# Kernel tuning notes

Measured on AMD Instinct MI355X. Metric: run time of the kernel, lower is better.

## Reference

```python
import jax, jax.numpy as jnp
import numpy as np

NB_LAYERS, KSIZE = 4, 5
DILATIONS = [1, 2, 4, 8]
NEG_SLOPE = 0.1
BN_EPS = 1e-5


def _cont_conv(times, feats, mask, dilation, p):
    """One ContConv1d layer: causal gather of time-diffs -> kernel MLP -> weighted aggregate + skip + BN."""
    k1W, k1b, k2W, k2b, k3W, k3b, skipW, skipb, gamma, beta = p
    bs, L, Cin = feats.shape
    Cout = skipW.shape[1]
    lags = jnp.arange(KSIZE) * dilation                    # (K,) include_zero_lag=True -> lag 0 included
    idx = jnp.arange(L)[None, :] - lags[:, None]           # (K, L) causal neighbor indices
    valid = idx >= 0
    idx_c = jnp.clip(idx, 0, L - 1)
    g_times = times[:, idx_c]                              # (bs, K, L)
    g_feats = feats[:, idx_c, :]                           # (bs, K, L, Cin)
    g_mask = (mask[:, idx_c] & valid[None] & mask[:, None, :]).astype(feats.dtype)
    dt = (times[:, None, :] - g_times) * g_mask            # (bs, K, L) zeroed where invalid
    # kernel MLP: scalar time-diff -> (Cin, Cout) mixing matrix
    h = jax.nn.leaky_relu(dt[..., None] @ k1W + k1b, NEG_SLOPE)
    h = jax.nn.leaky_relu(h @ k2W + k2b, NEG_SLOPE)
    kv = (h @ k3W + k3b).reshape(bs, KSIZE, L, Cin, Cout) * g_mask[..., None, None]
    out = jnp.einsum('bklc,bklcd->bld', g_feats, kv)       # aggregate over taps and input channels
    out = out + feats @ skipW + skipb                      # 1x1-conv skip connection
    mu = out.mean((0, 1))                                  # BatchNorm1d (training-mode batch stats)
    var = out.var((0, 1))
    return (out - mu) * jax.lax.rsqrt(var + BN_EPS) * gamma + beta


def _ccnn_forward(event_times, event_types, emb, k1W, k1b, k2W, k2b, k3W, k3b, skipW, skipb, gamma, beta):
    bs = event_times.shape[0]
    emb = emb.at[0].set(0.0)                               # padding_idx = 0
    times = jnp.concatenate([jnp.zeros((bs, 1), event_times.dtype), event_times], axis=1)
    bos = jnp.full((bs, 1), jnp.max(event_types) + 1, dtype=event_types.dtype)
    types = jnp.concatenate([bos, event_types], axis=1)
    mask = times != 0                                      # BOS (t=0) masked, as in the original
    enc = emb[types]                                       # (bs, L+1, C)
    for i in range(NB_LAYERS):
        p = (k1W[i], k1b[i], k2W[i], k2b[i], k3W[i], k3b[i], skipW[i], skipb[i], gamma[i], beta[i])
        enc = jax.nn.leaky_relu(_cont_conv(times, enc, mask, DILATIONS[i], p), NEG_SLOPE)
    return enc


def setup_inputs() -> dict:
    key = jax.random.key(0)
    ks = jax.random.split(key, 12)
    bs, L, C, H, num_types = 8, 2048, 32, 16, 100
    s = 0.05
    gaps = jax.random.uniform(ks[0], (bs, L)) * 0.1 + 0.01
    times = jnp.cumsum(gaps, axis=1)                       # strictly increasing positive event times
    types = jax.random.randint(ks[1], (bs, L), 0, num_types) + 1   # 1..num_types
    pad = jnp.arange(L) >= int(0.9 * L)
    times = jnp.where(pad[None, :], 0.0, times).astype(jnp.float32)
    types = jnp.where(pad[None, :], 0, types).astype(jnp.int32)
    return {
        'event_times': times,
        'event_types': types,
        'emb': jax.random.normal(ks[2], (num_types + 2, C)) * s,
        'k1W': jax.random.normal(ks[3], (NB_LAYERS, 1, H)) * s,
        'k1b': jnp.zeros((NB_LAYERS, H)),
        'k2W': jax.random.normal(ks[4], (NB_LAYERS, H, H)) * s,
        'k2b': jnp.zeros((NB_LAYERS, H)),
        'k3W': jax.random.normal(ks[5], (NB_LAYERS, H, C * C)) * s,
        'k3b': jnp.zeros((NB_LAYERS, C * C)),
        'skipW': jax.random.normal(ks[6], (NB_LAYERS, C, C)) * s,
        'skipb': jnp.zeros((NB_LAYERS, C)),
        'gamma': jnp.ones((NB_LAYERS, C)),
        'beta': jnp.zeros((NB_LAYERS, C)),
    }


def reference(event_times, event_types, emb, k1W, k1b, k2W, k2b, k3W, k3b, skipW, skipb, gamma, beta):
    return _ccnn_forward(event_times, event_types, emb, k1W, k1b, k2W, k2b, k3W, k3b, skipW, skipb, gamma, beta)
```

## Files before the change

### kernel.cpp

```cpp
#include <hip/hip_runtime.h>
#include <stdint.h>

#define NB_LAYERS 4
#define KSIZE 5
#define BSZ 8
#define LIN 2048
#define LSEQ 2049
#define CCH 32
#define HCH 16
#define MROWS (BSZ*LSEQ)
#define NTILES ((MROWS+15)/16)
#define KDIM 576
#define NEG 0.1f
#define BNEPS 1e-5f
#define NWAVEMAX 256
#define CONVGRID 205
#define CONVBLK 320

typedef _Float16 h2v __attribute__((ext_vector_type(2)));
typedef _Float16 h8v __attribute__((ext_vector_type(8)));
typedef float    f4v __attribute__((ext_vector_type(4)));

union H8 { h8v v; h2v h[4]; };

static __device__ __forceinline__ h2v mkh2(float a, float b) {
  h2v r; r[0] = (_Float16)a; r[1] = (_Float16)b; return r;
}

__global__ __launch_bounds__(256) void prep_kernel(
    const float* __restrict__ k3W, const float* __restrict__ k3b,
    const float* __restrict__ skipW, _Float16* __restrict__ Wt,
    const int* __restrict__ types, int* __restrict__ wavemax,
    float* __restrict__ stats) {
  int id = blockIdx.x * blockDim.x + threadIdx.x;

  if (id < NB_LAYERS * 64) stats[id] = 0.f;

  if (id < BSZ * LIN) {
    int v = types[id];
#pragma unroll
    for (int off = 32; off; off >>= 1) v = max(v, __shfl_xor(v, off, 64));
    if ((threadIdx.x & 63) == 0) wavemax[id >> 6] = v;
  }

  {
    int layer = id / (CCH * KDIM);
    int rem = id % (CCH * KDIM);
    int n = rem / KDIM;
    int k = rem % KDIM;
    float val;
    if (k < 512)      { int h = k >> 5, c = k & 31; val = k3W[layer*16384 + h*1024 + c*32 + n]; }
    else if (k < 544) { int c = k - 512;            val = k3b[layer*1024 + c*32 + n]; }
    else              { int c = k - 544;            val = skipW[layer*1024 + c*32 + n]; }
    Wt[id] = (_Float16)val;
  }
}

template<int MODE>
__global__ __launch_bounds__(CONVBLK) void conv_kernel(
    const float* __restrict__ enc_in,
    const int*   __restrict__ types,
    const float* __restrict__ emb,
    const int*   __restrict__ wavemax,
    float* __restrict__ enc_out,
    const float* __restrict__ etimes,
    const float* __restrict__ k1Wp, const float* __restrict__ k1bp,
    const float* __restrict__ k2Wp, const float* __restrict__ k2bp,
    const _Float16* __restrict__ Wt,
    const float* __restrict__ stats_prev, float* __restrict__ stats_out,
    const float* __restrict__ gamma_prev, const float* __restrict__ beta_prev,
    int dil)
{
  __shared__ float sst[64];
  __shared__ alignas(16) float sW[304];
  __shared__ h8v swh[CONVBLK/64 * KSIZE * 16 * 2];

  const int tid  = threadIdx.x;
  const int lane = tid & 63;
  const int wv   = tid >> 6;
  const int m    = lane & 15;
  const int q    = lane >> 4;

  if (tid < 64) sst[tid] = 0.f;
  if (tid < 16) { sW[tid] = k1Wp[tid]; sW[16 + tid] = k1bp[tid]; sW[32 + tid] = k2bp[tid]; }
  if (tid >= 64 && tid < 64 + 256) sW[48 + tid - 64] = k2Wp[tid - 64];
  __syncthreads();

  float sc8[8], ob8[8];
  if (MODE == 1) {
    const float inv = 1.f / (float)MROWS;
#pragma unroll
    for (int j = 0; j < 8; j++) {
      int c = q * 8 + j;
      float mu = stats_prev[c] * inv;
      float var = stats_prev[32 + c] * inv - mu * mu;
      float sc = gamma_prev[c] * rsqrtf(var + BNEPS);
      sc8[j] = sc; ob8[j] = beta_prev[c] - mu * sc;
    }
  }

  const _Float16* wb0 = Wt + m * KDIM + q * 8;
  const _Float16* wb1 = Wt + (m + 16) * KDIM + q * 8;

  const int tile = blockIdx.x * (CONVBLK / 64) + wv;
  int row = tile * 16 + m;
  bool rvalid = row < MROWS;
  int rowc = min(row, MROWS - 1);
  int b = rowc / LSEQ, pos = rowc % LSEQ;
  float t_l = (pos == 0) ? 0.f : etimes[b * LIN + pos - 1];
  bool mask_l = rvalid && (t_l != 0.f);

  int bosv = 0;
  if (MODE == 0) {
    if (__ballot(pos == 0)) {
      const int4* wm = (const int4*)wavemax;
      int mx = 0;
#pragma unroll 4
      for (int i = 0; i < NWAVEMAX / 4; i++) {
        int4 v = wm[i];
        mx = max(mx, max(max(v.x, v.y), max(v.z, v.w)));
      }
      bosv = mx + 1;
    }
  }

  h2v fh[KSIZE][4];
  h2v fself[4];
  float Fb[8];
#pragma unroll
  for (int jj = 0; jj < 8; jj++) Fb[jj] = 0.f;

#pragma unroll
  for (int tap = 0; tap < KSIZE; tap++) {
    int j = pos - tap * dil;
    int jc = max(j, 0);
    float t_j = (jc == 0) ? 0.f : etimes[b * LIN + jc - 1];
    bool gm = mask_l && (j >= 0) && (t_j != 0.f);

    float fv[8];
    if (MODE == 0) {
      int tl = 0;
      if (jc > 0) tl = types[b * LIN + jc - 1];
      int t = (jc == 0) ? ((tap == 0) ? bosv : 0) : tl;
      const float* ep = emb + t * CCH + q * 8;
      float4 eA = *(const float4*)(ep);
      float4 eB = *(const float4*)(ep + 4);
      float zf = (t != 0) ? 1.f : 0.f;
      fv[0]=eA.x*zf; fv[1]=eA.y*zf; fv[2]=eA.z*zf; fv[3]=eA.w*zf;
      fv[4]=eB.x*zf; fv[5]=eB.y*zf; fv[6]=eB.z*zf; fv[7]=eB.w*zf;
    } else {
      const float* fp = enc_in + (b * LSEQ + jc) * CCH + q * 8;
      float4 fA = *(const float4*)(fp);
      float4 fB = *(const float4*)(fp + 4);
      fv[0]=fA.x; fv[1]=fA.y; fv[2]=fA.z; fv[3]=fA.w;
      fv[4]=fB.x; fv[5]=fB.y; fv[6]=fB.z; fv[7]=fB.w;
#pragma unroll
      for (int jj = 0; jj < 8; jj++) {
        float x = fmaf(fv[jj], sc8[jj], ob8[jj]);
        fv[jj] = fmaxf(x, NEG * x);
      }
    }

    if (tap == 0) {
      float rv = rvalid ? 1.f : 0.f;
#pragma unroll
      for (int p2 = 0; p2 < 4; p2++) fself[p2] = mkh2(fv[2*p2] * rv, fv[2*p2+1] * rv);
    }
    float g = gm ? 1.f : 0.f;
#pragma unroll
    for (int jj = 0; jj < 8; jj++) Fb[jj] += g * fv[jj];
#pragma unroll
    for (int p2 = 0; p2 < 4; p2++) fh[tap][p2] = mkh2(fv[2*p2], fv[2*p2+1]);
  }

#pragma unroll
  for (int rep = 0; rep < 2; rep++) {
    const int jt = rep ? (KSIZE - 1) : (lane >> 4);
    const bool act = rep ? (lane < 16) : true;
    int j2 = pos - jt * dil;
    int jc2 = max(j2, 0);
    float tj2 = (jc2 == 0) ? 0.f : etimes[b * LIN + jc2 - 1];
    bool g2 = act && mask_l && (j2 >= 0) && (tj2 != 0.f);
    float dt = g2 ? (t_l - tj2) : 0.f;

    H8 w0, w1;
    if (__ballot(g2)) {
      const f4v* k1wv = (const f4v*)&sW[0];
      const f4v* k1bv = (const f4v*)&sW[16];
      const f4v* k2bv = (const f4v*)&sW[32];
      float h1[HCH], h2[HCH];
#pragma unroll
      for (int h4 = 0; h4 < 4; h4++) {
        f4v cw = k1wv[h4], cb = k1bv[h4], c2 = k2bv[h4];
#pragma unroll
        for (int r = 0; r < 4; r++) {
          float x = fmaf(dt, cw[r], cb[r]);
          h1[h4*4+r] = fmaxf(x, NEG * x);
          h2[h4*4+r] = c2[r];
        }
      }
#pragma unroll
      for (int hp = 0; hp < HCH; hp++) {
        float hv = h1[hp];
        const f4v* kk = (const f4v*)&sW[48 + hp * 16];
#pragma unroll
        for (int h4 = 0; h4 < 4; h4++) {
          f4v c = kk[h4];
#pragma unroll
          for (int r = 0; r < 4; r++) h2[h4*4+r] = fmaf(hv, c[r], h2[h4*4+r]);
        }
      }
      float g = g2 ? 1.f : 0.f;
#pragma unroll
      for (int p2 = 0; p2 < 4; p2++) {
        float a0 = h2[2*p2];     a0 = fmaxf(a0, NEG * a0) * g;
        float a1 = h2[2*p2+1];   a1 = fmaxf(a1, NEG * a1) * g;
        w0.h[p2] = mkh2(a0, a1);
        float b0 = h2[8+2*p2];   b0 = fmaxf(b0, NEG * b0) * g;
        float b1 = h2[8+2*p2+1]; b1 = fmaxf(b1, NEG * b1) * g;
        w1.h[p2] = mkh2(b0, b1);
      }
    } else {
#pragma unroll
      for (int p2 = 0; p2 < 4; p2++) { w0.h[p2] = mkh2(0.f, 0.f); w1.h[p2] = mkh2(0.f, 0.f); }
    }
    if (act) {
      int base = ((wv * KSIZE + jt) * 16 + m) * 2;
      swh[base] = w0.v; swh[base + 1] = w1.v;
    }
  }
  __syncthreads();

  h2v wh[KSIZE][8];
#pragma unroll
  for (int tap = 0; tap < KSIZE; tap++) {
    int base = ((wv * KSIZE + tap) * 16 + m) * 2;
    H8 a0, a1; a0.v = swh[base]; a1.v = swh[base + 1];
#pragma unroll
    for (int p2 = 0; p2 < 4; p2++) { wh[tap][p2] = a0.h[p2]; wh[tap][4+p2] = a1.h[p2]; }
  }

  f4v acc0 = {0.f, 0.f, 0.f, 0.f};
  f4v acc1 = {0.f, 0.f, 0.f, 0.f};

#pragma unroll
  for (int ks = 0; ks < 16; ks++) {
    H8 bf0, bf1, af;
    bf0.v = *(const h8v*)(wb0 + ks * 32);
    bf1.v = *(const h8v*)(wb1 + ks * 32);
    h2v u0 = mkh2(0.f,0.f), u1 = mkh2(0.f,0.f), u2 = mkh2(0.f,0.f), u3 = mkh2(0.f,0.f);
#pragma unroll
    for (int tap = 0; tap < KSIZE; tap++) {
      _Float16 w = wh[tap][ks >> 1][ks & 1];
      h2v wd; wd[0] = w; wd[1] = w;
      u0 += wd * fh[tap][0];
      u1 += wd * fh[tap][1];
      u2 += wd * fh[tap][2];
      u3 += wd * fh[tap][3];
    }
    af.h[0] = u0; af.h[1] = u1; af.h[2] = u2; af.h[3] = u3;
    acc0 = __builtin_amdgcn_mfma_f32_16x16x32_f16(af.v, bf0.v, acc0, 0, 0, 0);
    acc1 = __builtin_amdgcn_mfma_f32_16x16x32_f16(af.v, bf1.v, acc1, 0, 0, 0);
  }
  {
    H8 bf0, bf1, af;
    bf0.v = *(const h8v*)(wb0 + 512);
    bf1.v = *(const h8v*)(wb1 + 512);
#pragma unroll
    for (int p2 = 0; p2 < 4; p2++) af.h[p2] = mkh2(Fb[2*p2], Fb[2*p2+1]);
    acc0 = __builtin_amdgcn_mfma_f32_16x16x32_f16(af.v, bf0.v, acc0, 0, 0, 0);
    acc1 = __builtin_amdgcn_mfma_f32_16x16x32_f16(af.v, bf1.v, acc1, 0, 0, 0);
  }
  {
    H8 bf0, bf1, af;
    bf0.v = *(const h8v*)(wb0 + 544);
    bf1.v = *(const h8v*)(wb1 + 544);
    af.h[0] = fself[0]; af.h[1] = fself[1]; af.h[2] = fself[2]; af.h[3] = fself[3];
    acc0 = __builtin_amdgcn_mfma_f32_16x16x32_f16(af.v, bf0.v, acc0, 0, 0, 0);
    acc1 = __builtin_amdgcn_mfma_f32_16x16x32_f16(af.v, bf1.v, acc1, 0, 0, 0);
  }

  float s0 = 0.f, s1 = 0.f, s2 = 0.f, s3 = 0.f;
#pragma unroll
  for (int r = 0; r < 4; r++) {
    float v0 = acc0[r], v1 = acc1[r];
    s0 += v0; s1 += v0 * v0; s2 += v1; s3 += v1 * v1;
    int rd = tile * 16 + q * 4 + r;
    if (rd < MROWS) {
      enc_out[rd * CCH + m] = v0;
      enc_out[rd * CCH + 16 + m] = v1;
    }
  }
  s0 += __shfl_xor(s0, 16, 64); s0 += __shfl_xor(s0, 32, 64);
  s1 += __shfl_xor(s1, 16, 64); s1 += __shfl_xor(s1, 32, 64);
  s2 += __shfl_xor(s2, 16, 64); s2 += __shfl_xor(s2, 32, 64);
  s3 += __shfl_xor(s3, 16, 64); s3 += __shfl_xor(s3, 32, 64);
  if (q == 0) {
    atomicAdd(&sst[m], s0);
    atomicAdd(&sst[32 + m], s1);
    atomicAdd(&sst[16 + m], s2);
    atomicAdd(&sst[48 + m], s3);
  }
  __syncthreads();
  if (tid < 64) atomicAdd(&stats_out[tid], sst[tid]);
}

__global__ __launch_bounds__(256) void bn_kernel(
    const float* __restrict__ x, float* __restrict__ out,
    const float* __restrict__ stats,
    const float* __restrict__ gamma, const float* __restrict__ beta) {
  int id = blockIdx.x * blockDim.x + threadIdx.x;
  int c = id & 31;
  const float inv = 1.f / (float)MROWS;
  float mu = stats[c] * inv;
  float var = stats[32 + c] * inv - mu * mu;
  float sc = gamma[c] * rsqrtf(var + BNEPS);
  float v = fmaf(x[id], sc, beta[c] - mu * sc);
  out[id] = fmaxf(v, NEG * v);
}

extern "C" void kernel_launch(void* const* d_in, const int* in_sizes, int n_in,
                              void* d_out, int out_size, void* d_ws, size_t ws_size,
                              hipStream_t stream) {
  (void)in_sizes; (void)n_in; (void)out_size; (void)ws_size;
  const float* event_times = (const float*)d_in[0];
  const int*   event_types = (const int*)d_in[1];
  const float* emb   = (const float*)d_in[2];
  const float* k1W   = (const float*)d_in[3];
  const float* k1b   = (const float*)d_in[4];
  const float* k2W   = (const float*)d_in[5];
  const float* k2b   = (const float*)d_in[6];
  const float* k3W   = (const float*)d_in[7];
  const float* k3b   = (const float*)d_in[8];
  const float* skipW = (const float*)d_in[9];
  const float* gamma = (const float*)d_in[11];
  const float* beta  = (const float*)d_in[12];

  float* enc_a = (float*)d_ws;
  float* enc_b = enc_a + (size_t)MROWS * CCH;
  float* stats = enc_b + (size_t)MROWS * CCH;
  int*   wavemax = (int*)(stats + NB_LAYERS * 64);
  _Float16* Wt = (_Float16*)(((uintptr_t)(wavemax + NWAVEMAX) + 255) & ~(uintptr_t)255);

  prep_kernel<<<288, 256, 0, stream>>>(k3W, k3b, skipW, Wt, event_types, wavemax, stats);

  conv_kernel<0><<<CONVGRID, CONVBLK, 0, stream>>>(
      nullptr, event_types, emb, wavemax, enc_b, event_times,
      k1W, k1b, k2W, k2b, Wt, nullptr, stats, nullptr, nullptr, 1);

  const int dils[NB_LAYERS] = {1, 2, 4, 8};
  float* bufs[2] = {enc_a, enc_b};
  for (int i = 1; i < NB_LAYERS; i++) {
    const float* cin = bufs[i & 1];
    float* cout = bufs[(i + 1) & 1];
    conv_kernel<1><<<CONVGRID, CONVBLK, 0, stream>>>(
        cin, nullptr, nullptr, nullptr, cout, event_times,
        k1W + i * HCH, k1b + i * HCH, k2W + i * HCH * HCH, k2b + i * HCH,
        Wt + (size_t)i * CCH * KDIM,
        stats + (i - 1) * 64, stats + i * 64,
        gamma + (i - 1) * CCH, beta + (i - 1) * CCH, dils[i]);
  }
  bn_kernel<<<2049, 256, 0, stream>>>(enc_a, (float*)d_out,
      stats + 3 * 64, gamma + 3 * CCH, beta + 3 * CCH);
}
```

Measured before the change: 152.4 us.

## Fuse weight prep into first conv layer and stage MFMA weights in LDS

Removes the separate prep kernel. The first conv launch now repacks layer-0 weights into shared memory in MFMA fragment order and writes the packed weights for layers 1-3 to global memory. It also computes the max type per wave and stores per-block BN partials instead of using atomics. Later layers copy their packed fragments into LDS and read B operands from there, all gathers are hoisted ahead of compute for memory-level parallelism, and the accumulators are split into two interleaved chains. This saves one launch and some global weight traffic, at the cost of redundant per-block weight decoding in layer 0 and more LDS use, which may lower occupancy.

```diff
diff --git a/kernel.cpp b/kernel.cpp
--- a/kernel.cpp
+++ b/kernel.cpp
@@ -10,12 +10,12 @@
 #define HCH 16
 #define MROWS (BSZ*LSEQ)
 #define NTILES ((MROWS+15)/16)
-#define KDIM 576
 #define NEG 0.1f
 #define BNEPS 1e-5f
-#define NWAVEMAX 256
 #define CONVGRID 205
 #define CONVBLK 320
+#define NFRAG 36
+#define WT_HALVES (NFRAG*64*8)
 
 typedef _Float16 h2v __attribute__((ext_vector_type(2)));
 typedef _Float16 h8v __attribute__((ext_vector_type(8)));
@@ -27,33 +27,16 @@
   h2v r; r[0] = (_Float16)a; r[1] = (_Float16)b; return r;
 }
 
-__global__ __launch_bounds__(256) void prep_kernel(
-    const float* __restrict__ k3W, const float* __restrict__ k3b,
-    const float* __restrict__ skipW, _Float16* __restrict__ Wt,
-    const int* __restrict__ types, int* __restrict__ wavemax,
-    float* __restrict__ stats) {
-  int id = blockIdx.x * blockDim.x + threadIdx.x;
-
-  if (id < NB_LAYERS * 64) stats[id] = 0.f;
-
-  if (id < BSZ * LIN) {
-    int v = types[id];
-#pragma unroll
-    for (int off = 32; off; off >>= 1) v = max(v, __shfl_xor(v, off, 64));
-    if ((threadIdx.x & 63) == 0) wavemax[id >> 6] = v;
-  }
-
-  {
-    int layer = id / (CCH * KDIM);
-    int rem = id % (CCH * KDIM);
-    int n = rem / KDIM;
-    int k = rem % KDIM;
-    float val;
-    if (k < 512)      { int h = k >> 5, c = k & 31; val = k3W[layer*16384 + h*1024 + c*32 + n]; }
-    else if (k < 544) { int c = k - 512;            val = k3b[layer*1024 + c*32 + n]; }
-    else              { int c = k - 544;            val = skipW[layer*1024 + c*32 + n]; }
-    Wt[id] = (_Float16)val;
-  }
+static __device__ __forceinline__ void wt_decode(
+    int g, const float* __restrict__ k3Wl, const float* __restrict__ k3bl,
+    const float* __restrict__ skipWl, int& halfidx, float& val) {
+  int n, k;
+  if (g < 16384)      { n = g & 31; int c = (g >> 5) & 31; int h = g >> 10; k = h * 32 + c; val = k3Wl[g]; }
+  else if (g < 17408) { int g2 = g - 16384; n = g2 & 31; int c = g2 >> 5; k = 512 + c; val = k3bl[g2]; }
+  else                { int g2 = g - 17408; n = g2 & 31; int c = g2 >> 5; k = 544 + c; val = skipWl[g2]; }
+  int m = n & 15, a = n >> 4, qq = (k >> 3) & 3, hh = k & 7;
+  int f = (k < 512) ? ((k >> 5) * 2 + a) : ((k < 544) ? (32 + a) : (34 + a));
+  halfidx = f * 512 + ((qq << 4) | m) * 8 + hh;
 }
 
 template<int MODE>
@@ -61,19 +44,26 @@
     const float* __restrict__ enc_in,
     const int*   __restrict__ types,
     const float* __restrict__ emb,
-    const int*   __restrict__ wavemax,
     float* __restrict__ enc_out,
     const float* __restrict__ etimes,
     const float* __restrict__ k1Wp, const float* __restrict__ k1bp,
     const float* __restrict__ k2Wp, const float* __restrict__ k2bp,
-    const _Float16* __restrict__ Wt,
-    const float* __restrict__ stats_prev, float* __restrict__ stats_out,
+    const float* __restrict__ k3W, const float* __restrict__ k3b,
+    const float* __restrict__ skipW,
+    _Float16* __restrict__ WtG,
+    const float* __restrict__ stats_prev,
+    const float* __restrict__ partials_prev,
+    float* __restrict__ stats_out,
+    float* __restrict__ partials_out,
+    float* __restrict__ stats_zero,
     const float* __restrict__ gamma_prev, const float* __restrict__ beta_prev,
     int dil)
 {
+  __shared__ h8v Wl[NFRAG * 64];
+  __shared__ h8v swh[(CONVBLK/64) * KSIZE * 16 * 2];
+  __shared__ alignas(16) float sW[304];
   __shared__ float sst[64];
-  __shared__ alignas(16) float sW[304];
-  __shared__ h8v swh[CONVBLK/64 * KSIZE * 16 * 2];
+  __shared__ float sbn[64];
 
   const int tid  = threadIdx.x;
   const int lane = tid & 63;
@@ -83,8 +73,37 @@
 
   if (tid < 64) sst[tid] = 0.f;
   if (tid < 16) { sW[tid] = k1Wp[tid]; sW[16 + tid] = k1bp[tid]; sW[32 + tid] = k2bp[tid]; }
-  if (tid >= 64 && tid < 64 + 256) sW[48 + tid - 64] = k2Wp[tid - 64];
+  if (tid >= 64) sW[48 + tid - 64] = k2Wp[tid - 64];
+
+  if (MODE == 0) {
+    if (blockIdx.x == 0 && tid < 192) stats_zero[tid] = 0.f;
+    for (int g = tid; g < WT_HALVES; g += CONVBLK) {
+      int hi; float val;
+      wt_decode(g, k3W, k3b, skipW, hi, val);
+      ((_Float16*)Wl)[hi] = (_Float16)val;
+    }
+    int id2 = blockIdx.x * CONVBLK + tid;
+    if (id2 < 3 * WT_HALVES) {
+      int layer = 1 + id2 / WT_HALVES;
+      int g = id2 - (layer - 1) * WT_HALVES;
+      int hi; float val;
+      wt_decode(g, k3W + layer * 16384, k3b + layer * 1024, skipW + layer * 1024, hi, val);
+      WtG[(layer - 1) * WT_HALVES + hi] = (_Float16)val;
+    }
+  } else {
+    const float4* src = (const float4*)WtG;
+    float4* dst = (float4*)Wl;
+    for (int i = tid; i < WT_HALVES / 8; i += CONVBLK) dst[i] = src[i];
+    if (partials_prev && tid < 64) sbn[tid] = 0.f;
+  }
   __syncthreads();
+
+  if (MODE == 1 && partials_prev) {
+    float v = 0.f;
+    for (int i = tid; i < CONVGRID * 64; i += CONVBLK) v += partials_prev[i];
+    atomicAdd(&sbn[tid & 63], v);
+    __syncthreads();
+  }
 
   float sc8[8], ob8[8];
   if (MODE == 1) {
@@ -92,15 +111,14 @@
 #pragma unroll
     for (int j = 0; j < 8; j++) {
       int c = q * 8 + j;
-      float mu = stats_prev[c] * inv;
-      float var = stats_prev[32 + c] * inv - mu * mu;
+      float s1 = partials_prev ? sbn[c]      : stats_prev[c];
+      float s2 = partials_prev ? sbn[32 + c] : stats_prev[32 + c];
+      float mu = s1 * inv;
+      float var = s2 * inv - mu * mu;
       float sc = gamma_prev[c] * rsqrtf(var + BNEPS);
       sc8[j] = sc; ob8[j] = beta_prev[c] - mu * sc;
     }
   }
-
-  const _Float16* wb0 = Wt + m * KDIM + q * 8;
-  const _Float16* wb1 = Wt + (m + 16) * KDIM + q * 8;
 
   const int tile = blockIdx.x * (CONVBLK / 64) + wv;
   int row = tile * 16 + m;
@@ -113,14 +131,40 @@
   int bosv = 0;
   if (MODE == 0) {
     if (__ballot(pos == 0)) {
-      const int4* wm = (const int4*)wavemax;
       int mx = 0;
-#pragma unroll 4
-      for (int i = 0; i < NWAVEMAX / 4; i++) {
-        int4 v = wm[i];
-        mx = max(mx, max(max(v.x, v.y), max(v.z, v.w)));
-      }
+#pragma unroll 8
+      for (int i = lane; i < BSZ * LIN; i += 64) mx = max(mx, types[i]);
+#pragma unroll
+      for (int off = 32; off; off >>= 1) mx = max(mx, __shfl_xor(mx, off, 64));
       bosv = mx + 1;
+    }
+  }
+
+  int jcs[KSIZE]; float tjv[KSIZE];
+#pragma unroll
+  for (int tap = 0; tap < KSIZE; tap++) {
+    int j = pos - tap * dil;
+    int jc = max(j, 0); jcs[tap] = jc;
+    tjv[tap] = (jc == 0) ? 0.f : etimes[b * LIN + jc - 1];
+  }
+  float4 fa[KSIZE], fbv[KSIZE];
+  int tts[KSIZE];
+  if (MODE == 0) {
+#pragma unroll
+    for (int tap = 0; tap < KSIZE; tap++) {
+      int jc = jcs[tap];
+      tts[tap] = (jc > 0) ? types[b * LIN + jc - 1] : ((tap == 0) ? bosv : 0);
+    }
+#pragma unroll
+    for (int tap = 0; tap < KSIZE; tap++) {
+      const float* ep = emb + tts[tap] * CCH + q * 8;
+      fa[tap] = *(const float4*)ep; fbv[tap] = *(const float4*)(ep + 4);
+    }
+  } else {
+#pragma unroll
+    for (int tap = 0; tap < KSIZE; tap++) {
+      const float* fp = enc_in + (b * LSEQ + jcs[tap]) * CCH + q * 8;
+      fa[tap] = *(const float4*)fp; fbv[tap] = *(const float4*)(fp + 4);
     }
   }
 
@@ -132,35 +176,20 @@
 
 #pragma unroll
   for (int tap = 0; tap < KSIZE; tap++) {
-    int j = pos - tap * dil;
-    int jc = max(j, 0);
-    float t_j = (jc == 0) ? 0.f : etimes[b * LIN + jc - 1];
-    bool gm = mask_l && (j >= 0) && (t_j != 0.f);
-
-    float fv[8];
+    bool gm = mask_l && (pos - tap * dil >= 0) && (tjv[tap] != 0.f);
+    float fv[8] = {fa[tap].x, fa[tap].y, fa[tap].z, fa[tap].w,
+                   fbv[tap].x, fbv[tap].y, fbv[tap].z, fbv[tap].w};
     if (MODE == 0) {
-      int tl = 0;
-      if (jc > 0) tl = types[b * LIN + jc - 1];
-      int t = (jc == 0) ? ((tap == 0) ? bosv : 0) : tl;
-      const float* ep = emb + t * CCH + q * 8;
-      float4 eA = *(const float4*)(ep);
-      float4 eB = *(const float4*)(ep + 4);
-      float zf = (t != 0) ? 1.f : 0.f;
-      fv[0]=eA.x*zf; fv[1]=eA.y*zf; fv[2]=eA.z*zf; fv[3]=eA.w*zf;
-      fv[4]=eB.x*zf; fv[5]=eB.y*zf; fv[6]=eB.z*zf; fv[7]=eB.w*zf;
+      float zf = (tts[tap] != 0) ? 1.f : 0.f;
+#pragma unroll
+      for (int jj = 0; jj < 8; jj++) fv[jj] *= zf;
     } else {
-      const float* fp = enc_in + (b * LSEQ + jc) * CCH + q * 8;
-      float4 fA = *(const float4*)(fp);
-      float4 fB = *(const float4*)(fp + 4);
-      fv[0]=fA.x; fv[1]=fA.y; fv[2]=fA.z; fv[3]=fA.w;
-      fv[4]=fB.x; fv[5]=fB.y; fv[6]=fB.z; fv[7]=fB.w;
 #pragma unroll
       for (int jj = 0; jj < 8; jj++) {
         float x = fmaf(fv[jj], sc8[jj], ob8[jj]);
         fv[jj] = fmaxf(x, NEG * x);
       }
     }
-
     if (tap == 0) {
       float rv = rvalid ? 1.f : 0.f;
 #pragma unroll
@@ -240,14 +269,13 @@
     for (int p2 = 0; p2 < 4; p2++) { wh[tap][p2] = a0.h[p2]; wh[tap][4+p2] = a1.h[p2]; }
   }
 
-  f4v acc0 = {0.f, 0.f, 0.f, 0.f};
-  f4v acc1 = {0.f, 0.f, 0.f, 0.f};
+  f4v aP = {0,0,0,0}, aQ = {0,0,0,0}, bP = {0,0,0,0}, bQ = {0,0,0,0};
 
 #pragma unroll
   for (int ks = 0; ks < 16; ks++) {
     H8 bf0, bf1, af;
-    bf0.v = *(const h8v*)(wb0 + ks * 32);
-    bf1.v = *(const h8v*)(wb1 + ks * 32);
+    bf0.v = Wl[(2*ks + 0) * 64 + lane];
+    bf1.v = Wl[(2*ks + 1) * 64 + lane];
     h2v u0 = mkh2(0.f,0.f), u1 = mkh2(0.f,0.f), u2 = mkh2(0.f,0.f), u3 = mkh2(0.f,0.f);
 #pragma unroll
     for (int tap = 0; tap < KSIZE; tap++) {
@@ -259,26 +287,33 @@
       u3 += wd * fh[tap][3];
     }
     af.h[0] = u0; af.h[1] = u1; af.h[2] = u2; af.h[3] = u3;
-    acc0 = __builtin_amdgcn_mfma_f32_16x16x32_f16(af.v, bf0.v, acc0, 0, 0, 0);
-    acc1 = __builtin_amdgcn_mfma_f32_16x16x32_f16(af.v, bf1.v, acc1, 0, 0, 0);
+    if (ks & 1) {
+      aQ = __builtin_amdgcn_mfma_f32_16x16x32_f16(af.v, bf0.v, aQ, 0, 0, 0);
+      bQ = __builtin_amdgcn_mfma_f32_16x16x32_f16(af.v, bf1.v, bQ, 0, 0, 0);
+    } else {
+      aP = __builtin_amdgcn_mfma_f32_16x16x32_f16(af.v, bf0.v, aP, 0, 0, 0);
+      bP = __builtin_amdgcn_mfma_f32_16x16x32_f16(af.v, bf1.v, bP, 0, 0, 0);
+    }
   }
   {
     H8 bf0, bf1, af;
-    bf0.v = *(const h8v*)(wb0 + 512);
-    bf1.v = *(const h8v*)(wb1 + 512);
+    bf0.v = Wl[32 * 64 + lane];
+    bf1.v = Wl[33 * 64 + lane];
 #pragma unroll
     for (int p2 = 0; p2 < 4; p2++) af.h[p2] = mkh2(Fb[2*p2], Fb[2*p2+1]);
-    acc0 = __builtin_amdgcn_mfma_f32_16x16x32_f16(af.v, bf0.v, acc0, 0, 0, 0);
-    acc1 = __builtin_amdgcn_mfma_f32_16x16x32_f16(af.v, bf1.v, acc1, 0, 0, 0);
+    aP = __builtin_amdgcn_mfma_f32_16x16x32_f16(af.v, bf0.v, aP, 0, 0, 0);
+    bP = __builtin_amdgcn_mfma_f32_16x16x32_f16(af.v, bf1.v, bP, 0, 0, 0);
   }
   {
     H8 bf0, bf1, af;
-    bf0.v = *(const h8v*)(wb0 + 544);
-    bf1.v = *(const h8v*)(wb1 + 544);
+    bf0.v = Wl[34 * 64 + lane];
+    bf1.v = Wl[35 * 64 + lane];
     af.h[0] = fself[0]; af.h[1] = fself[1]; af.h[2] = fself[2]; af.h[3] = fself[3];
-    acc0 = __builtin_amdgcn_mfma_f32_16x16x32_f16(af.v, bf0.v, acc0, 0, 0, 0);
-    acc1 = __builtin_amdgcn_mfma_f32_16x16x32_f16(af.v, bf1.v, acc1, 0, 0, 0);
-  }
+    aQ = __builtin_amdgcn_mfma_f32_16x16x32_f16(af.v, bf0.v, aQ, 0, 0, 0);
+    bQ = __builtin_amdgcn_mfma_f32_16x16x32_f16(af.v, bf1.v, bQ, 0, 0, 0);
+  }
+  f4v acc0 = aP + aQ;
+  f4v acc1 = bP + bQ;
 
   float s0 = 0.f, s1 = 0.f, s2 = 0.f, s3 = 0.f;
 #pragma unroll
@@ -302,7 +337,10 @@
     atomicAdd(&sst[48 + m], s3);
   }
   __syncthreads();
-  if (tid < 64) atomicAdd(&stats_out[tid], sst[tid]);
+  if (tid < 64) {
+    if (MODE == 0) partials_out[blockIdx.x * 64 + tid] = sst[tid];
+    else           atomicAdd(&stats_out[tid], sst[tid]);
+  }
 }
 
 __global__ __launch_bounds__(256) void bn_kernel(
@@ -339,27 +377,36 @@
   float* enc_a = (float*)d_ws;
   float* enc_b = enc_a + (size_t)MROWS * CCH;
   float* stats = enc_b + (size_t)MROWS * CCH;
-  int*   wavemax = (int*)(stats + NB_LAYERS * 64);
-  _Float16* Wt = (_Float16*)(((uintptr_t)(wavemax + NWAVEMAX) + 255) & ~(uintptr_t)255);
-
-  prep_kernel<<<288, 256, 0, stream>>>(k3W, k3b, skipW, Wt, event_types, wavemax, stats);
+  float* partials0 = stats + NB_LAYERS * 64;
+  _Float16* WtG = (_Float16*)(((uintptr_t)(partials0 + CONVGRID * 64) + 255) & ~(uintptr_t)255);
 
   conv_kernel<0><<<CONVGRID, CONVBLK, 0, stream>>>(
-      nullptr, event_types, emb, wavemax, enc_b, event_times,
-      k1W, k1b, k2W, k2b, Wt, nullptr, stats, nullptr, nullptr, 1);
-
-  const int dils[NB_LAYERS] = {1, 2, 4, 8};
-  float* bufs[2] = {enc_a, enc_b};
-  for (int i = 1; i < NB_LAYERS; i++) {
-    const float* cin = bufs[i & 1];
-    float* cout = bufs[(i + 1) & 1];
-    conv_kernel<1><<<CONVGRID, CONVBLK, 0, stream>>>(
-        cin, nullptr, nullptr, nullptr, cout, event_times,
-        k1W + i * HCH, k1b + i * HCH, k2W + i * HCH * HCH, k2b + i * HCH,
-        Wt + (size_t)i * CCH * KDIM,
-        stats + (i - 1) * 64, stats + i * 64,
-        gamma + (i - 1) * CCH, beta + (i - 1) * CCH, dils[i]);
-  }
+      nullptr, event_types, emb, enc_b, event_times,
+      k1W, k1b, k2W, k2b, k3W, k3b, skipW, WtG,
+      nullptr, nullptr, nullptr, partials0, stats + 64,
+      nullptr, nullptr, 1);
+
+  conv_kernel<1><<<CONVGRID, CONVBLK, 0, stream>>>(
+      enc_b, nullptr, nullptr, enc_a, event_times,
+      k1W + HCH, k1b + HCH, k2W + HCH*HCH, k2b + HCH,
+      nullptr, nullptr, nullptr, WtG + 0 * WT_HALVES,
+      nullptr, partials0, stats + 64, nullptr, nullptr,
+      gamma + 0 * CCH, beta + 0 * CCH, 2);
+
+  conv_kernel<1><<<CONVGRID, CONVBLK, 0, stream>>>(
+      enc_a, nullptr, nullptr, enc_b, event_times,
+      k1W + 2*HCH, k1b + 2*HCH, k2W + 2*HCH*HCH, k2b + 2*HCH,
+      nullptr, nullptr, nullptr, WtG + 1 * WT_HALVES,
+      stats + 64, nullptr, stats + 128, nullptr, nullptr,
+      gamma + 1 * CCH, beta + 1 * CCH, 4);
+
+  conv_kernel<1><<<CONVGRID, CONVBLK, 0, stream>>>(
+      enc_b, nullptr, nullptr, enc_a, event_times,
+      k1W + 3*HCH, k1b + 3*HCH, k2W + 3*HCH*HCH, k2b + 3*HCH,
+      nullptr, nullptr, nullptr, WtG + 2 * WT_HALVES,
+      stats + 128, nullptr, stats + 192, nullptr, nullptr,
+      gamma + 2 * CCH, beta + 2 * CCH, 8);
+
   bn_kernel<<<2049, 256, 0, stream>>>(enc_a, (float*)d_out,
-      stats + 3 * 64, gamma + 3 * CCH, beta + 3 * CCH);
+      stats + 192, gamma + 3 * CCH, beta + 3 * CCH);
 }
```

After: 165.6 us. 1.09x slower.
